# Optimization experiments

Hardware: AMD Instinct MI355X
Metric: run time of the kernel (lower is better)

Reference implementation:

```python
import jax, jax.numpy as jnp
import numpy as np

B, S, D, H = 4, 2048, 1024, 16
HD = D // H  # head_dim = 64


def setup_inputs() -> dict:
    key = jax.random.key(0)
    ks = jax.random.split(key, 5)
    hidden_states = jax.random.normal(ks[0], (B, S, D), dtype=jnp.float32)
    # GPT-2 Conv1D: out = x @ W + b, W shape [in, out]
    w_attn = jax.random.normal(ks[1], (D, 3 * D), dtype=jnp.float32) * 0.02
    b_attn = jnp.zeros((3 * D,), dtype=jnp.float32)
    w_proj = jax.random.normal(ks[2], (D, D), dtype=jnp.float32) * 0.02
    b_proj = jnp.zeros((D,), dtype=jnp.float32)
    return {"hidden_states": hidden_states, "w_attn": w_attn, "b_attn": b_attn,
            "w_proj": w_proj, "b_proj": b_proj}


def reference(hidden_states, w_attn, b_attn, w_proj, b_proj):
    b, s, d = hidden_states.shape
    qkv = hidden_states @ w_attn + b_attn                     # [B,S,3D]
    q, k, v = jnp.split(qkv, 3, axis=-1)
    # split heads -> [B,H,S,HD]
    def heads(x):
        return x.reshape(b, s, H, HD).transpose(0, 2, 1, 3)
    q, k, v = heads(q), heads(k), heads(v)
    # scaled dot product; GPT-2 divides by sqrt(head_dim)
    scores = jnp.einsum("bhqd,bhkd->bhqk", q, k) / jnp.sqrt(jnp.float32(HD))
    causal = jnp.tril(jnp.ones((s, s), dtype=bool))           # [S,S]
    neg = jnp.finfo(scores.dtype).min
    scores = jnp.where(causal[None, None, :, :], scores, neg)
    attn = jax.nn.softmax(scores, axis=-1)
    ctx = jnp.einsum("bhqk,bhkd->bhqd", attn, v)              # [B,H,S,HD]
    ctx = ctx.transpose(0, 2, 1, 3).reshape(b, s, d)          # merge heads
    return ctx @ w_proj + b_proj
```

## Files before the change

### kernel.cpp

```cpp
#include <hip/hip_runtime.h>
#include <hip/hip_bf16.h>

typedef __bf16 bf16;
typedef bf16 bf16x8 __attribute__((ext_vector_type(8)));
typedef bf16 bf16x4 __attribute__((ext_vector_type(4)));
typedef float f32x4 __attribute__((ext_vector_type(4)));

#define MFMA16(a, b, c) __builtin_amdgcn_mfma_f32_16x16x32_bf16(a, b, c, 0, 0, 0)

constexpr int Bn = 4, Sn = 2048, Dn = 1024, Hn = 16, HDn = 64;
constexpr int Mn = Bn * Sn;

__device__ __forceinline__ bf16x8 cvt8(float4 a, float4 b) {
  bf16x8 v = {(bf16)a.x, (bf16)a.y, (bf16)a.z, (bf16)a.w,
              (bf16)b.x, (bf16)b.y, (bf16)b.z, (bf16)b.w};
  return v;
}

__device__ __forceinline__ void load_lds16(const bf16* g, bf16* l) {
  __builtin_amdgcn_global_load_lds(
      (const __attribute__((address_space(1))) void*)g,
      (__attribute__((address_space(3))) void*)l, 16, 0, 0);
}

__global__ __launch_bounds__(256) void k_cvt(const float* __restrict__ in,
                                             bf16* __restrict__ out) {
  int i = blockIdx.x * 256 + threadIdx.x;
  const float4* p = (const float4*)in + (size_t)i * 2;
  float4 a = p[0], b = p[1];
  *((bf16x8*)out + i) = cvt8(a, b);
}

__global__ __launch_bounds__(256) void k_transpose_cvt(const float* __restrict__ in,
                                                       bf16* __restrict__ out,
                                                       int K, int N) {
  __shared__ alignas(16) bf16 t[64][72];
  const int n0 = blockIdx.x * 64, k0 = blockIdx.y * 64;
  const int tid = threadIdx.x;
  {
    int row = tid >> 2;
    int c16 = (tid & 3) * 16;
    const float* src = in + (size_t)(k0 + row) * N + n0 + c16;
    float4 f0 = ((const float4*)src)[0];
    float4 f1 = ((const float4*)src)[1];
    float4 f2 = ((const float4*)src)[2];
    float4 f3 = ((const float4*)src)[3];
    *(bf16x8*)&t[row][c16] = cvt8(f0, f1);
    *(bf16x8*)&t[row][c16 + 8] = cvt8(f2, f3);
  }
  __syncthreads();
#pragma unroll
  for (int i = 0; i < 2; i++) {
    int c = tid + i * 256;
    int nrow = c >> 3, kcol8 = (c & 7) * 8;
    bf16x8 v;
#pragma unroll
    for (int j = 0; j < 8; j++) v[j] = t[kcol8 + j][nrow];
    *(bf16x8*)(out + (size_t)(n0 + nrow) * K + k0 + kcol8) = v;
  }
}


__global__ __launch_bounds__(256) void k_gemm_qkv(const bf16* __restrict__ A,
                                                  const bf16* __restrict__ BT,
                                                  const float* __restrict__ bias,
                                                  bf16* __restrict__ Qo,
                                                  bf16* __restrict__ Ko,
                                                  bf16* __restrict__ Vt) {
  __shared__ alignas(16) bf16 la[128 * 32];
  __shared__ alignas(16) bf16 lb[128 * 32];
  const int tid = threadIdx.x;
  const int w = tid >> 6, lane = tid & 63, l15 = lane & 15, quad = lane >> 4;
  const int wm = w >> 1, wn = w & 1;
  const int m0 = blockIdx.y * 128, n0 = blockIdx.x * 128;
  const int lrow = lane >> 2, lcol = (lane & 3) * 8;

  f32x4 acc[4][4];
#pragma unroll
  for (int i = 0; i < 4; i++)
#pragma unroll
    for (int j = 0; j < 4; j++) acc[i][j] = f32x4{0.f, 0.f, 0.f, 0.f};

  for (int k0 = 0; k0 < 1024; k0 += 32) {
    __syncthreads();
    load_lds16(A + (size_t)(m0 + w * 16 + lrow) * 1024 + k0 + lcol, &la[w * 512]);
    load_lds16(A + (size_t)(m0 + 64 + w * 16 + lrow) * 1024 + k0 + lcol, &la[(w + 4) * 512]);
    load_lds16(BT + (size_t)(n0 + w * 16 + lrow) * 1024 + k0 + lcol, &lb[w * 512]);
    load_lds16(BT + (size_t)(n0 + 64 + w * 16 + lrow) * 1024 + k0 + lcol, &lb[(w + 4) * 512]);
    __syncthreads();
    bf16x8 af[4], bfr[4];
#pragma unroll
    for (int i = 0; i < 4; i++)
      af[i] = *(const bf16x8*)&la[(wm * 64 + i * 16 + l15) * 32 + quad * 8];
#pragma unroll
    for (int j = 0; j < 4; j++)
      bfr[j] = *(const bf16x8*)&lb[(wn * 64 + j * 16 + l15) * 32 + quad * 8];
#pragma unroll
    for (int i = 0; i < 4; i++)
#pragma unroll
      for (int j = 0; j < 4; j++) acc[i][j] = MFMA16(af[i], bfr[j], acc[i][j]);
  }

#pragma unroll
  for (int j = 0; j < 4; j++) {
    int ng = n0 + wn * 64 + j * 16 + l15;
    float bs = bias[ng];
    int which = ng >> 10;
    int nloc = ng & 1023, hh = nloc >> 6, hd = nloc & 63;
#pragma unroll
    for (int i = 0; i < 4; i++) {
      int mg0 = m0 + wm * 64 + i * 16 + quad * 4;
      int bb = mg0 >> 11, ss = mg0 & 2047;
      if (which == 2) {
        bf16x4 v;
#pragma unroll
        for (int r = 0; r < 4; r++) v[r] = (bf16)(acc[i][j][r] + bs);
        *(bf16x4*)&Vt[((size_t)(bb * Hn + hh) * HDn + hd) * Sn + ss] = v;
      } else {
        bf16* dst = which ? Ko : Qo;
#pragma unroll
        for (int r = 0; r < 4; r++)
          dst[((size_t)(bb * Hn + hh) * Sn + ss + r) * HDn + hd] =
              (bf16)(acc[i][j][r] + bs);
      }
    }
  }
}

__global__ __launch_bounds__(256) void k_gemm_proj(const bf16* __restrict__ A,
                                                   const bf16* __restrict__ BT,
                                                   const float* __restrict__ bias,
                                                   float* __restrict__ out) {
  __shared__ alignas(16) bf16 la[128 * 32];
  __shared__ alignas(16) bf16 lb[128 * 32];
  const int tid = threadIdx.x;
  const int w = tid >> 6, lane = tid & 63, l15 = lane & 15, quad = lane >> 4;
  const int wm = w >> 1, wn = w & 1;
  const int m0 = blockIdx.y * 128, n0 = blockIdx.x * 128;
  const int lrow = lane >> 2, lcol = (lane & 3) * 8;

  f32x4 acc[4][4];
#pragma unroll
  for (int i = 0; i < 4; i++)
#pragma unroll
    for (int j = 0; j < 4; j++) acc[i][j] = f32x4{0.f, 0.f, 0.f, 0.f};

  for (int k0 = 0; k0 < 1024; k0 += 32) {
    __syncthreads();
    load_lds16(A + (size_t)(m0 + w * 16 + lrow) * 1024 + k0 + lcol, &la[w * 512]);
    load_lds16(A + (size_t)(m0 + 64 + w * 16 + lrow) * 1024 + k0 + lcol, &la[(w + 4) * 512]);
    load_lds16(BT + (size_t)(n0 + w * 16 + lrow) * 1024 + k0 + lcol, &lb[w * 512]);
    load_lds16(BT + (size_t)(n0 + 64 + w * 16 + lrow) * 1024 + k0 + lcol, &lb[(w + 4) * 512]);
    __syncthreads();
    bf16x8 af[4], bfr[4];
#pragma unroll
    for (int i = 0; i < 4; i++)
      af[i] = *(const bf16x8*)&la[(wm * 64 + i * 16 + l15) * 32 + quad * 8];
#pragma unroll
    for (int j = 0; j < 4; j++)
      bfr[j] = *(const bf16x8*)&lb[(wn * 64 + j * 16 + l15) * 32 + quad * 8];
#pragma unroll
    for (int i = 0; i < 4; i++)
#pragma unroll
      for (int j = 0; j < 4; j++) acc[i][j] = MFMA16(af[i], bfr[j], acc[i][j]);
  }

#pragma unroll
  for (int j = 0; j < 4; j++) {
    int ng = n0 + wn * 64 + j * 16 + l15;
    float bs = bias[ng];
#pragma unroll
    for (int i = 0; i < 4; i++) {
      int mg0 = m0 + wm * 64 + i * 16 + quad * 4;
#pragma unroll
      for (int r = 0; r < 4; r++)
        out[(size_t)(mg0 + r) * 1024 + ng] = acc[i][j][r] + bs;
    }
  }
}

__global__ __launch_bounds__(256) void k_attn(const bf16* __restrict__ Q,
                                              const bf16* __restrict__ Kv,
                                              const bf16* __restrict__ Vtg,
                                              bf16* __restrict__ ctx) {
  __shared__ alignas(16) bf16 kt[64][72];
  __shared__ alignas(16) bf16 vtT[64][72];
  __shared__ alignas(16) bf16 plds[4][16][68];

  const int bh = blockIdx.x;
  const int p = blockIdx.y;
  const int bb = bh >> 4, hh = bh & 15;
  const int tid = threadIdx.x;
  const int w = tid >> 6, lane = tid & 63, l15 = lane & 15, quad = lane >> 4;
  const size_t base = (size_t)bh * Sn * HDn;
  const int srow = tid >> 2, sc16 = (tid & 3) * 16;

  bf16x8 ones_f;
#pragma unroll
  for (int e = 0; e < 8; e++) ones_f[e] = (l15 == 0) ? (bf16)1.0f : (bf16)0.0f;

#pragma unroll
  for (int half = 0; half < 2; half++) {
    const int qt = half ? (31 - p) : p;
    const int q0 = qt * 64;
    const int qw = q0 + w * 16;

    bf16x8 aq[2];
#pragma unroll
    for (int c = 0; c < 2; c++) {
      bf16x8 v = *(const bf16x8*)(Q + base + (size_t)(qw + l15) * 64 + c * 32 +
                                  quad * 8);
#pragma unroll
      for (int e = 0; e < 8; e++) v[e] = (bf16)((float)v[e] * 0.125f);
      aq[c] = v;
    }

    f32x4 o[4];
    f32x4 o4;
#pragma unroll
    for (int h = 0; h < 4; h++) o[h] = f32x4{0.f, 0.f, 0.f, 0.f};
    o4 = f32x4{0.f, 0.f, 0.f, 0.f};

    for (int kb = 0; kb < q0 + 64; kb += 64) {
      __syncthreads();
      {
        const bf16* kg = Kv + base + (size_t)(kb + srow) * 64 + sc16;
        *(bf16x8*)&kt[srow][sc16] = *(const bf16x8*)kg;
        *(bf16x8*)&kt[srow][sc16 + 8] = *(const bf16x8*)(kg + 8);
        const bf16* vg = Vtg + ((size_t)bh * 64 + srow) * Sn + kb + sc16;
        *(bf16x8*)&vtT[srow][sc16] = *(const bf16x8*)vg;
        *(bf16x8*)&vtT[srow][sc16 + 8] = *(const bf16x8*)(vg + 8);
      }
      __syncthreads();
      if (kb > qw + 15) continue;

      f32x4 st[4];
#pragma unroll
      for (int ks = 0; ks < 4; ks++) {
        f32x4 a = f32x4{0.f, 0.f, 0.f, 0.f};
        bf16x8 b0 = *(const bf16x8*)&kt[ks * 16 + l15][quad * 8];
        bf16x8 b1 = *(const bf16x8*)&kt[ks * 16 + l15][32 + quad * 8];
        a = MFMA16(aq[0], b0, a);
        a = MFMA16(aq[1], b1, a);
        st[ks] = a;
      }

      if (kb + 63 > qw) {
#pragma unroll
        for (int ks = 0; ks < 4; ks++)
#pragma unroll
          for (int r = 0; r < 4; r++) {
            int qg = qw + quad * 4 + r;
            int kg = kb + ks * 16 + l15;
            if (kg > qg) st[ks][r] = -1e30f;
          }
      }

#pragma unroll
      for (int r = 0; r < 4; r++)
#pragma unroll
        for (int ks = 0; ks < 4; ks++)
          plds[w][quad * 4 + r][ks * 16 + l15] = (bf16)__expf(st[ks][r]);

      asm volatile("s_waitcnt lgkmcnt(0)" ::: "memory");
      bf16x8 ap0 = *(const bf16x8*)&plds[w][l15][quad * 8];
      bf16x8 ap1 = *(const bf16x8*)&plds[w][l15][32 + quad * 8];
#pragma unroll
      for (int h = 0; h < 4; h++) {
        bf16x8 bv0 = *(const bf16x8*)&vtT[h * 16 + l15][quad * 8];
        bf16x8 bv1 = *(const bf16x8*)&vtT[h * 16 + l15][32 + quad * 8];
        o[h] = MFMA16(ap0, bv0, o[h]);
        o[h] = MFMA16(ap1, bv1, o[h]);
      }
      o4 = MFMA16(ap0, ones_f, o4);
      o4 = MFMA16(ap1, ones_f, o4);
    }

#pragma unroll
    for (int r = 0; r < 4; r++) {
      float s = __shfl(o4[r], lane & 48, 64);
      float inv = 1.f / fmaxf(s, 1e-20f);
      int qg = qw + quad * 4 + r;
      size_t ob = ((size_t)(bb * Sn + qg)) * Dn + hh * HDn;
#pragma unroll
      for (int h = 0; h < 4; h++)
        ctx[ob + h * 16 + l15] = (bf16)(o[h][r] * inv);
    }
  }
}

extern "C" void kernel_launch(void* const* d_in, const int* in_sizes, int n_in,
                              void* d_out, int out_size, void* d_ws, size_t ws_size,
                              hipStream_t stream) {
  const float* hidden = (const float*)d_in[0];
  const float* w_attn = (const float*)d_in[1];
  const float* b_attn = (const float*)d_in[2];
  const float* w_proj = (const float*)d_in[3];
  const float* b_proj = (const float*)d_in[4];
  float* out = (float*)d_out;

  bf16* ws = (bf16*)d_ws;
  const size_t QKV_ELEMS = (size_t)Bn * Hn * Sn * HDn;
  bf16* Qb = ws;
  bf16* Kb = Qb + QKV_ELEMS;
  bf16* Vt = Kb + QKV_ELEMS;
  bf16* ctx = Vt + QKV_ELEMS;
  bf16* Xb = ctx;
  bf16* wattnT = ctx + (size_t)Mn * Dn;
  bf16* wprojT = wattnT + (size_t)Dn * 3 * Dn;

  k_cvt<<<4096, 256, 0, stream>>>(hidden, Xb);
  k_transpose_cvt<<<dim3(48, 16), 256, 0, stream>>>(w_attn, wattnT, 1024, 3072);
  k_transpose_cvt<<<dim3(16, 16), 256, 0, stream>>>(w_proj, wprojT, 1024, 1024);
  k_gemm_qkv<<<dim3(24, 64), 256, 0, stream>>>(Xb, wattnT, b_attn, Qb, Kb, Vt);
  k_attn<<<dim3(64, 16), 256, 0, stream>>>(Qb, Kb, Vt, ctx);
  k_gemm_proj<<<dim3(8, 64), 256, 0, stream>>>(ctx, wprojT, b_proj, out);
}
```

Measured before the change: 263.6 us.

## Rewrite causal attention kernel with 32x32 MFMA, register-resident P, and double-buffered async loads

Rewrites the attention kernel so each wave handles 32 query rows using 32x32x16 bf16 MFMAs. It computes S^T so that P stays in registers via packed bf16 conversion and permlane32 swaps, removing the LDS round trip for P. The row sum is now accumulated in scalar registers rather than through an extra MFMA against a ones vector. K and V tiles are prefetched with direct global-to-LDS loads into XOR-swizzled double buffers. The grid now needs 16 q-tiles of 128 in reverse order instead of paired 64-row tiles, and the launch-side grid change is not visible, so this may not match the launch config.

```diff
diff --git a/kernel.cpp b/kernel.cpp
--- a/kernel.cpp
+++ b/kernel.cpp
@@ -5,8 +5,11 @@
 typedef bf16 bf16x8 __attribute__((ext_vector_type(8)));
 typedef bf16 bf16x4 __attribute__((ext_vector_type(4)));
 typedef float f32x4 __attribute__((ext_vector_type(4)));
+typedef float f32x16 __attribute__((ext_vector_type(16)));
+typedef unsigned int uint2v __attribute__((ext_vector_type(2)));
 
 #define MFMA16(a, b, c) __builtin_amdgcn_mfma_f32_16x16x32_bf16(a, b, c, 0, 0, 0)
+#define MFMA32(a, b, c) __builtin_amdgcn_mfma_f32_32x32x16_bf16(a, b, c, 0, 0, 0)
 
 constexpr int Bn = 4, Sn = 2048, Dn = 1024, Hn = 16, HDn = 64;
 constexpr int Mn = Bn * Sn;
@@ -21,6 +24,12 @@
   __builtin_amdgcn_global_load_lds(
       (const __attribute__((address_space(1))) void*)g,
       (__attribute__((address_space(3))) void*)l, 16, 0, 0);
+}
+
+__device__ __forceinline__ unsigned cvt_pk_bf16(float lo, float hi) {
+  unsigned r;
+  asm("v_cvt_pk_bf16_f32 %0, %1, %2" : "=v"(r) : "v"(lo), "v"(hi));
+  return r;
 }
 
 __global__ __launch_bounds__(256) void k_cvt(const float* __restrict__ in,
@@ -183,109 +192,125 @@
                                               const bf16* __restrict__ Kv,
                                               const bf16* __restrict__ Vtg,
                                               bf16* __restrict__ ctx) {
-  __shared__ alignas(16) bf16 kt[64][72];
-  __shared__ alignas(16) bf16 vtT[64][72];
-  __shared__ alignas(16) bf16 plds[4][16][68];
+  __shared__ alignas(16) bf16 kl[2][64 * 64];
+  __shared__ alignas(16) bf16 vl[2][64 * 64];
 
   const int bh = blockIdx.x;
-  const int p = blockIdx.y;
+  const int qt = 15 - blockIdx.y;
   const int bb = bh >> 4, hh = bh & 15;
   const int tid = threadIdx.x;
-  const int w = tid >> 6, lane = tid & 63, l15 = lane & 15, quad = lane >> 4;
+  const int w = tid >> 6, lane = tid & 63, l31 = lane & 31, hi = lane >> 5;
   const size_t base = (size_t)bh * Sn * HDn;
-  const int srow = tid >> 2, sc16 = (tid & 3) * 16;
-
-  bf16x8 ones_f;
-#pragma unroll
-  for (int e = 0; e < 8; e++) ones_f[e] = (l15 == 0) ? (bf16)1.0f : (bf16)0.0f;
-
-#pragma unroll
-  for (int half = 0; half < 2; half++) {
-    const int qt = half ? (31 - p) : p;
-    const int q0 = qt * 64;
-    const int qw = q0 + w * 16;
-
-    bf16x8 aq[2];
-#pragma unroll
-    for (int c = 0; c < 2; c++) {
-      bf16x8 v = *(const bf16x8*)(Q + base + (size_t)(qw + l15) * 64 + c * 32 +
-                                  quad * 8);
-#pragma unroll
-      for (int e = 0; e < 8; e++) v[e] = (bf16)((float)v[e] * 0.125f);
-      aq[c] = v;
-    }
-
-    f32x4 o[4];
-    f32x4 o4;
-#pragma unroll
-    for (int h = 0; h < 4; h++) o[h] = f32x4{0.f, 0.f, 0.f, 0.f};
-    o4 = f32x4{0.f, 0.f, 0.f, 0.f};
-
-    for (int kb = 0; kb < q0 + 64; kb += 64) {
-      __syncthreads();
-      {
-        const bf16* kg = Kv + base + (size_t)(kb + srow) * 64 + sc16;
-        *(bf16x8*)&kt[srow][sc16] = *(const bf16x8*)kg;
-        *(bf16x8*)&kt[srow][sc16 + 8] = *(const bf16x8*)(kg + 8);
-        const bf16* vg = Vtg + ((size_t)bh * 64 + srow) * Sn + kb + sc16;
-        *(bf16x8*)&vtT[srow][sc16] = *(const bf16x8*)vg;
-        *(bf16x8*)&vtT[srow][sc16 + 8] = *(const bf16x8*)(vg + 8);
+  const int q0 = qt * 128 + w * 32;
+  const int kend = qt * 128 + 128;
+
+  const int r0 = tid >> 3, s0 = tid & 7;
+  const int ksw = (s0 ^ (r0 & 7)) << 3;
+  const bf16* Krow = Kv + base + (size_t)r0 * 64 + ksw;
+  const bf16* Vrow0 = Vtg + ((size_t)bh * 64 + r0) * Sn + ksw;
+  const bf16* Vrow1 = Vtg + ((size_t)bh * 64 + r0 + 32) * Sn + ksw;
+  const int sw7 = l31 & 7;
+
+  bf16x8 qf[4];
+#pragma unroll
+  for (int c = 0; c < 4; c++) {
+    bf16x8 v = *(const bf16x8*)(Q + base + (size_t)(q0 + l31) * 64 + c * 16 + hi * 8);
+#pragma unroll
+    for (int e = 0; e < 8; e++) v[e] = (bf16)((float)v[e] * 0.125f);
+    qf[c] = v;
+  }
+
+  f32x16 o0, o1;
+#pragma unroll
+  for (int e = 0; e < 16; e++) { o0[e] = 0.f; o1[e] = 0.f; }
+  float dsum = 0.f;
+
+  load_lds16(Krow, &kl[0][w * 512]);
+  load_lds16(Krow + 32 * 64, &kl[0][2048 + w * 512]);
+  load_lds16(Vrow0, &vl[0][w * 512]);
+  load_lds16(Vrow1, &vl[0][2048 + w * 512]);
+
+  int cur = 0;
+  for (int kb = 0; kb < kend; kb += 64) {
+    __syncthreads();
+    if (kb + 64 < kend) {
+      const int nk = kb + 64;
+      load_lds16(Krow + (size_t)nk * 64, &kl[cur ^ 1][w * 512]);
+      load_lds16(Krow + (size_t)(nk + 32) * 64, &kl[cur ^ 1][2048 + w * 512]);
+      load_lds16(Vrow0 + nk, &vl[cur ^ 1][w * 512]);
+      load_lds16(Vrow1 + nk, &vl[cur ^ 1][2048 + w * 512]);
+    }
+    if (kb <= q0 + 31) {
+      const bf16* klc = kl[cur];
+      const bf16* vlc = vl[cur];
+#pragma unroll
+      for (int sub = 0; sub < 2; sub++) {
+        const int ks0 = kb + sub * 32;
+        if (ks0 > q0 + 31) break;
+        f32x16 st;
+#pragma unroll
+        for (int e = 0; e < 16; e++) st[e] = 0.f;
+#pragma unroll
+        for (int c = 0; c < 4; c++) {
+          const int row = sub * 32 + l31;
+          bf16x8 kf = *(const bf16x8*)&klc[row * 64 + (((2 * c + hi) ^ sw7) << 3)];
+          st = MFMA32(kf, qf[c], st);
+        }
+        if (ks0 == q0) {
+#pragma unroll
+          for (int r = 0; r < 16; r++) {
+            int krel = (r & 3) + 8 * (r >> 2) + 4 * hi;
+            if (krel > l31) st[r] = -1e30f;
+          }
+        }
+#pragma unroll
+        for (int r = 0; r < 16; r++) {
+          st[r] = __expf(st[r]);
+          dsum += st[r];
+        }
+#pragma unroll
+        for (int c2 = 0; c2 < 2; c2++) {
+          unsigned wa0 = cvt_pk_bf16(st[8 * c2 + 0], st[8 * c2 + 1]);
+          unsigned wa1 = cvt_pk_bf16(st[8 * c2 + 2], st[8 * c2 + 3]);
+          unsigned wb0 = cvt_pk_bf16(st[8 * c2 + 4], st[8 * c2 + 5]);
+          unsigned wb1 = cvt_pk_bf16(st[8 * c2 + 6], st[8 * c2 + 7]);
+          unsigned pw0, pw1, pw2, pw3;
+#if __has_builtin(__builtin_amdgcn_permlane32_swap)
+          uint2v sw0 = __builtin_amdgcn_permlane32_swap(wa0, wb0, false, false);
+          uint2v sw1 = __builtin_amdgcn_permlane32_swap(wa1, wb1, false, false);
+          pw0 = sw0.x; pw1 = sw1.x; pw2 = sw0.y; pw3 = sw1.y;
+#else
+          unsigned xa0 = __shfl_xor((int)wa0, 32, 64), xb0 = __shfl_xor((int)wb0, 32, 64);
+          unsigned xa1 = __shfl_xor((int)wa1, 32, 64), xb1 = __shfl_xor((int)wb1, 32, 64);
+          pw0 = hi ? xb0 : wa0; pw1 = hi ? xb1 : wa1;
+          pw2 = hi ? wb0 : xa0; pw3 = hi ? wb1 : xa1;
+#endif
+          union { unsigned u[4]; bf16x8 v; } pb;
+          pb.u[0] = pw0; pb.u[1] = pw1; pb.u[2] = pw2; pb.u[3] = pw3;
+          const int vs = sub * 4 + 2 * c2;
+          bf16x8 vf0 = *(const bf16x8*)&vlc[l31 * 64 + (((vs + hi) ^ sw7) << 3)];
+          o0 = MFMA32(vf0, pb.v, o0);
+          bf16x8 vf1 = *(const bf16x8*)&vlc[(32 + l31) * 64 + (((vs + hi) ^ sw7) << 3)];
+          o1 = MFMA32(vf1, pb.v, o1);
+        }
       }
-      __syncthreads();
-      if (kb > qw + 15) continue;
-
-      f32x4 st[4];
-#pragma unroll
-      for (int ks = 0; ks < 4; ks++) {
-        f32x4 a = f32x4{0.f, 0.f, 0.f, 0.f};
-        bf16x8 b0 = *(const bf16x8*)&kt[ks * 16 + l15][quad * 8];
-        bf16x8 b1 = *(const bf16x8*)&kt[ks * 16 + l15][32 + quad * 8];
-        a = MFMA16(aq[0], b0, a);
-        a = MFMA16(aq[1], b1, a);
-        st[ks] = a;
-      }
-
-      if (kb + 63 > qw) {
-#pragma unroll
-        for (int ks = 0; ks < 4; ks++)
-#pragma unroll
-          for (int r = 0; r < 4; r++) {
-            int qg = qw + quad * 4 + r;
-            int kg = kb + ks * 16 + l15;
-            if (kg > qg) st[ks][r] = -1e30f;
-          }
-      }
-
-#pragma unroll
-      for (int r = 0; r < 4; r++)
-#pragma unroll
-        for (int ks = 0; ks < 4; ks++)
-          plds[w][quad * 4 + r][ks * 16 + l15] = (bf16)__expf(st[ks][r]);
-
-      asm volatile("s_waitcnt lgkmcnt(0)" ::: "memory");
-      bf16x8 ap0 = *(const bf16x8*)&plds[w][l15][quad * 8];
-      bf16x8 ap1 = *(const bf16x8*)&plds[w][l15][32 + quad * 8];
-#pragma unroll
-      for (int h = 0; h < 4; h++) {
-        bf16x8 bv0 = *(const bf16x8*)&vtT[h * 16 + l15][quad * 8];
-        bf16x8 bv1 = *(const bf16x8*)&vtT[h * 16 + l15][32 + quad * 8];
-        o[h] = MFMA16(ap0, bv0, o[h]);
-        o[h] = MFMA16(ap1, bv1, o[h]);
-      }
-      o4 = MFMA16(ap0, ones_f, o4);
-      o4 = MFMA16(ap1, ones_f, o4);
-    }
-
+    }
+    cur ^= 1;
+  }
+
+  float tot = dsum + __shfl_xor(dsum, 32, 64);
+  float inv = 1.f / fmaxf(tot, 1e-20f);
+  size_t ob = ((size_t)(bb * Sn + q0 + l31)) * Dn + hh * HDn + hi * 4;
+#pragma unroll
+  for (int g = 0; g < 4; g++) {
+    bf16x4 v0, v1;
 #pragma unroll
     for (int r = 0; r < 4; r++) {
-      float s = __shfl(o4[r], lane & 48, 64);
-      float inv = 1.f / fmaxf(s, 1e-20f);
-      int qg = qw + quad * 4 + r;
-      size_t ob = ((size_t)(bb * Sn + qg)) * Dn + hh * HDn;
-#pragma unroll
-      for (int h = 0; h < 4; h++)
-        ctx[ob + h * 16 + l15] = (bf16)(o[h][r] * inv);
-    }
+      v0[r] = (bf16)(o0[4 * g + r] * inv);
+      v1[r] = (bf16)(o1[4 * g + r] * inv);
+    }
+    *(bf16x4*)&ctx[ob + g * 8] = v0;
+    *(bf16x4*)&ctx[ob + 32 + g * 8] = v1;
   }
 }
 
```

Result: faster. 248.9 us (-5.6%).
